# Kernel optimization log

Hardware: AMD Instinct MI355X
Metric: run time of the kernel (lower is better)

Reference implementation:

```python
import jax, jax.numpy as jnp
import numpy as np

K = 8  # 2^3 kernel offsets for kernel-size-2, stride-2 transposed conv in 3D (HYPER_CUBE)
HID = 64


def sp_convT(x, W, parent, kofs):
    """Sparse generative transposed conv via kernel map.
    x: [Nin, Cin]; W: [K, Cin, Cout]; parent: [Nout] int; kofs: [Nout] int in [0,K).
    out[j] = x[parent[j]] @ W[kofs[j]].
    """
    xg = x[parent]  # [Nout, Cin] gather
    out = jnp.zeros((parent.shape[0], W.shape[2]), dtype=x.dtype)
    for k in range(K):  # fixed small structural loop over kernel offsets
        out = out + jnp.where((kofs == k)[:, None], xg @ W[k], jnp.zeros((), x.dtype))
    return out


def setup_inputs() -> dict:
    key = jax.random.key(0)
    ks = jax.random.split(key, 12)
    Ns = [5000, 20000, 80000, 320000]
    sc_i = 1.0 / np.sqrt(64)
    inp = {
        'x0': jax.random.normal(ks[0], (Ns[0], 64), jnp.float32),
        'x1': jax.random.normal(ks[1], (Ns[1], 64), jnp.float32),
        'x2': jax.random.normal(ks[2], (Ns[2], 64), jnp.float32),
        'W_i': jax.random.normal(ks[3], (K, 64, 4 * HID), jnp.float32) * sc_i,
        'W_h': jax.random.normal(ks[4], (K, HID, 4 * HID), jnp.float32) * sc_i,
        'W_c': jax.random.normal(ks[5], (K, HID, HID), jnp.float32) * sc_i,
        'parent0': jax.random.randint(ks[6], (Ns[1],), 0, Ns[0], jnp.int32),
        'kofs0': jax.random.randint(ks[7], (Ns[1],), 0, K, jnp.int32),
        'parent1': jax.random.randint(ks[8], (Ns[2],), 0, Ns[1], jnp.int32),
        'kofs1': jax.random.randint(ks[9], (Ns[2],), 0, K, jnp.int32),
        'parent2': jax.random.randint(ks[10], (Ns[3],), 0, Ns[2], jnp.int32),
        'kofs2': jax.random.randint(ks[11], (Ns[3],), 0, K, jnp.int32),
    }
    return inp


def reference(x0, x1, x2, W_i, W_h, W_c, parent0, kofs0, parent1, kofs1, parent2, kofs2):
    xs = [x0, x1, x2]
    parents = [parent0, parent1, parent2]
    kofss = [kofs0, kofs1, kofs2]
    hx = jnp.zeros((x0.shape[0], HID), dtype=x0.dtype)
    cx = jnp.zeros((x0.shape[0], HID), dtype=x0.dtype)
    for t in range(3):  # coder_num timesteps (structural loop)
        p, ko = parents[t], kofss[t]
        cx = sp_convT(cx, W_c, p, ko)                                   # upsample cell state
        gates = sp_convT(hx, W_h, p, ko) + sp_convT(xs[t], W_i, p, ko)  # [Nout, 4*HID]
        in_g, fg, cg, og = jnp.split(gates, 4, axis=1)
        in_g = jax.nn.sigmoid(in_g)
        fg = jax.nn.sigmoid(fg)
        cg = jax.nn.sigmoid(cg)  # NOTE: original uses sigmoid (not tanh) for cell_gate
        og = jax.nn.sigmoid(og)
        cx = fg * cx + in_g * cg
        hx = og * jnp.tanh(cx)
    return hx
```

## Files before the change

kernel.cpp:

```cpp
#include <hip/hip_runtime.h>


#define KNUM 8
#define TM 32
#define STEP_THREADS 256

typedef __attribute__((ext_vector_type(8))) _Float16 f16x8;
typedef __attribute__((ext_vector_type(4))) float f32x4;

__device__ __forceinline__ float fsig(float x) {
  return __builtin_amdgcn_rcpf(1.0f + __expf(-x));
}
__device__ __forceinline__ float ftanh_(float x) {
  float e = __expf(2.0f * x);
  return 1.0f - 2.0f * __builtin_amdgcn_rcpf(e + 1.0f);
}
__device__ __forceinline__ f16x8 to_h8(float4 a, float4 b) {
  f16x8 r;
  r[0] = (_Float16)a.x; r[1] = (_Float16)a.y; r[2] = (_Float16)a.z; r[3] = (_Float16)a.w;
  r[4] = (_Float16)b.x; r[5] = (_Float16)b.y; r[6] = (_Float16)b.z; r[7] = (_Float16)b.w;
  return r;
}

__global__ void prep_kernel(const float* __restrict__ Wi, const float* __restrict__ Wh,
                            const float* __restrict__ Wc,
                            const float* __restrict__ x0, const float* __restrict__ x1,
                            const float* __restrict__ x2, int ne0, int ne1, int ne2,
                            _Float16* __restrict__ WgT, _Float16* __restrict__ WcT,
                            _Float16* __restrict__ x0f, _Float16* __restrict__ x1f,
                            _Float16* __restrict__ x2f,
                            int* __restrict__ counts, int* __restrict__ cursor) {
  int tid = blockIdx.x * blockDim.x + threadIdx.x;
  int stride = gridDim.x * blockDim.x;
  if (tid < 3 * KNUM) { counts[tid] = 0; cursor[tid] = 0; }
  for (int idx = tid; idx < KNUM * 256 * 128; idx += stride) {
    int k  = idx >> 15;
    int co = (idx >> 7) & 255;
    int ci = idx & 127;
    float v = (ci < 64) ? Wh[(k * 64 + ci) * 256 + co]
                        : Wi[(k * 64 + ci - 64) * 256 + co];
    WgT[idx] = (_Float16)v;
  }
  for (int idx = tid; idx < KNUM * 64 * 64; idx += stride) {
    int k  = idx >> 12;
    int co = (idx >> 6) & 63;
    int ci = idx & 63;
    WcT[idx] = (_Float16)Wc[(k * 64 + ci) * 64 + co];
  }
  for (int i = tid; i < (ne0 >> 3); i += stride) {
    float4 a = ((const float4*)x0)[2 * i], b = ((const float4*)x0)[2 * i + 1];
    ((f16x8*)x0f)[i] = to_h8(a, b);
  }
  for (int i = tid; i < (ne1 >> 3); i += stride) {
    float4 a = ((const float4*)x1)[2 * i], b = ((const float4*)x1)[2 * i + 1];
    ((f16x8*)x1f)[i] = to_h8(a, b);
  }
  for (int i = tid; i < (ne2 >> 3); i += stride) {
    float4 a = ((const float4*)x2)[2 * i], b = ((const float4*)x2)[2 * i + 1];
    ((f16x8*)x2f)[i] = to_h8(a, b);
  }
}

__device__ __forceinline__ void seg_select(int b, int& seg, int& rb, int& nb) {
  if (b < 32)       { seg = 0; rb = b;       nb = 32;  }
  else if (b < 160) { seg = 1; rb = b - 32;  nb = 128; }
  else              { seg = 2; rb = b - 160; nb = 352; }
}

__global__ void count_all_kernel(const int* __restrict__ k0, int n0,
                                 const int* __restrict__ k1, int n1,
                                 const int* __restrict__ k2, int n2,
                                 int* __restrict__ counts) {
  int seg, rb, nb;
  seg_select(blockIdx.x, seg, rb, nb);
  const int* kp = seg == 0 ? k0 : seg == 1 ? k1 : k2;
  int n = seg == 0 ? n0 : seg == 1 ? n1 : n2;
  int* cbase = counts + seg * KNUM;
  __shared__ int h[KNUM];
  if (threadIdx.x < KNUM) h[threadIdx.x] = 0;
  __syncthreads();
  for (int i = rb * blockDim.x + threadIdx.x; i < n; i += nb * blockDim.x)
    atomicAdd(&h[kp[i]], 1);
  __syncthreads();
  if (threadIdx.x < KNUM) atomicAdd(&cbase[threadIdx.x], h[threadIdx.x]);
}

__global__ void scatter_all_kernel(const int* __restrict__ k0, const int* __restrict__ p0, int n0,
                                   int* __restrict__ o0, int* __restrict__ q0,
                                   const int* __restrict__ k1, const int* __restrict__ p1, int n1,
                                   int* __restrict__ o1, int* __restrict__ q1,
                                   const int* __restrict__ k2, const int* __restrict__ p2, int n2,
                                   int* __restrict__ o2, int* __restrict__ q2,
                                   const int* __restrict__ counts, int* __restrict__ cursor) {
  int seg, rb, nb;
  seg_select(blockIdx.x, seg, rb, nb);
  const int* kp = seg == 0 ? k0 : seg == 1 ? k1 : k2;
  const int* pp = seg == 0 ? p0 : seg == 1 ? p1 : p2;
  int n = seg == 0 ? n0 : seg == 1 ? n1 : n2;
  int* order  = seg == 0 ? o0 : seg == 1 ? o1 : o2;
  int* porder = seg == 0 ? q0 : seg == 1 ? q1 : q2;

  __shared__ int h[KNUM], base[KNUM];
  if (threadIdx.x < KNUM) h[threadIdx.x] = 0;
  __syncthreads();
  int chunk = (n + nb - 1) / nb;
  int c0 = rb * chunk;
  int c1 = min(n, c0 + chunk);
  for (int i = c0 + threadIdx.x; i < c1; i += blockDim.x)
    atomicAdd(&h[kp[i]], 1);
  __syncthreads();
  if (threadIdx.x < KNUM) {
    int offk = 0;
    for (int k = 0; k < (int)threadIdx.x; ++k) offk += counts[seg * KNUM + k];
    base[threadIdx.x] = offk + atomicAdd(&cursor[seg * KNUM + threadIdx.x], h[threadIdx.x]);
    h[threadIdx.x] = 0;
  }
  __syncthreads();
  for (int i = c0 + threadIdx.x; i < c1; i += blockDim.x) {
    int k = kp[i];
    int pos = base[k] + atomicAdd(&h[k], 1);
    order[pos] = i;
    porder[pos] = pp[i];
  }
}

template <bool FIRST, bool LAST>
__global__ __launch_bounds__(STEP_THREADS)
void lstm_step_kernel(const _Float16* __restrict__ xf, const _Float16* __restrict__ h_in,
                      const _Float16* __restrict__ c_in,
                      const int* __restrict__ order, const int* __restrict__ porder,
                      const int* __restrict__ counts,
                      const _Float16* __restrict__ WgT, const _Float16* __restrict__ WcT,
                      float* __restrict__ out32, _Float16* __restrict__ h16,
                      _Float16* __restrict__ c16, int bpk) {
  __shared__ __align__(16) _Float16 A[TM][136];
  __shared__ __align__(16) _Float16 Cg[TM][72];
  __shared__ int jidx[TM];

  const int kb = blockIdx.x & 7;
  const int bi = blockIdx.x >> 3;
  int cnt = 0, off = 0;
#pragma unroll
  for (int k = 0; k < KNUM; ++k) {
    int c = counts[k];
    if (k < kb) off += c;
    if (k == kb) cnt = c;
  }
  const int ntiles = (cnt + TM - 1) / TM;
  if (bi >= ntiles) return;

  const int lane = threadIdx.x & 63;
  const int wc   = threadIdx.x >> 6;
  const int l15  = lane & 15;
  const int kg   = lane >> 4;

  f16x8 bg[4][4];
  f16x8 bc[2];
  {
    const _Float16* wgp = WgT + (size_t)kb * (256 * 128);
#pragma unroll
    for (int g = 0; g < 4; ++g)
#pragma unroll
      for (int ks = (FIRST ? 2 : 0); ks < 4; ++ks)
        bg[g][ks] = *(const f16x8*)(wgp + (size_t)(64 * g + 16 * wc + l15) * 128 + ks * 32 + kg * 8);
    if constexpr (!FIRST) {
      const _Float16* wcp = WcT + (size_t)kb * (64 * 64);
#pragma unroll
      for (int ks = 0; ks < 2; ++ks)
        bc[ks] = *(const f16x8*)(wcp + (size_t)(16 * wc + l15) * 64 + ks * 32 + kg * 8);
    }
  }

  const int gr  = threadIdx.x >> 3;
  const int gq8 = threadIdx.x & 7;

  int cj, cp; bool cv;
  int nj, np; bool nv;
  f16x8 sx{}, sh{}, sc{};

  auto idx_load = [&](int tt, int& j_, int& p_, bool& v_) {
    int grow = tt * TM + gr;
    v_ = (tt < ntiles) && (grow < cnt);
    j_ = -1; p_ = 0;
    if (v_) {
      if (gq8 == 0) j_ = order[off + grow];
      p_ = porder[off + grow];
    }
  };
  auto rows_load = [&](int p_, bool v_) {
    if (v_) {
      sx = *(const f16x8*)(xf + (size_t)p_ * 64 + gq8 * 8);
      if constexpr (!FIRST) {
        sh = *(const f16x8*)(h_in + (size_t)p_ * 64 + gq8 * 8);
        sc = *(const f16x8*)(c_in + (size_t)p_ * 64 + gq8 * 8);
      }
    } else {
      sx = f16x8{};
      if constexpr (!FIRST) { sh = f16x8{}; sc = f16x8{}; }
    }
  };

  idx_load(bi, cj, cp, cv);
  rows_load(cp, cv);
  idx_load(bi + bpk, nj, np, nv);

  for (int t = bi; t < ntiles; t += bpk) {
    __syncthreads();
    if (gq8 == 0) jidx[gr] = cj;
    *(f16x8*)&A[gr][64 + gq8 * 8] = sx;
    if constexpr (!FIRST) {
      *(f16x8*)&A[gr][gq8 * 8]  = sh;
      *(f16x8*)&Cg[gr][gq8 * 8] = sc;
    }
    __syncthreads();

    rows_load(np, nv);
    cj = nj;
    idx_load(t + 2 * bpk, nj, np, nv);

    f32x4 aG[2][4];
    f32x4 aC[2];
#pragma unroll
    for (int rf = 0; rf < 2; ++rf) {
#pragma unroll
      for (int g = 0; g < 4; ++g) aG[rf][g] = f32x4{0.f, 0.f, 0.f, 0.f};
      aC[rf] = f32x4{0.f, 0.f, 0.f, 0.f};
    }
#pragma unroll
    for (int ks = (FIRST ? 2 : 0); ks < 4; ++ks) {
#pragma unroll
      for (int rf = 0; rf < 2; ++rf) {
        f16x8 a = *(const f16x8*)&A[16 * rf + l15][ks * 32 + kg * 8];
        aG[rf][0] = __builtin_amdgcn_mfma_f32_16x16x32_f16(a, bg[0][ks], aG[rf][0], 0, 0, 0);
        aG[rf][1] = __builtin_amdgcn_mfma_f32_16x16x32_f16(a, bg[1][ks], aG[rf][1], 0, 0, 0);
        aG[rf][2] = __builtin_amdgcn_mfma_f32_16x16x32_f16(a, bg[2][ks], aG[rf][2], 0, 0, 0);
        aG[rf][3] = __builtin_amdgcn_mfma_f32_16x16x32_f16(a, bg[3][ks], aG[rf][3], 0, 0, 0);
      }
    }
    if constexpr (!FIRST) {
#pragma unroll
      for (int ks = 0; ks < 2; ++ks) {
#pragma unroll
        for (int rf = 0; rf < 2; ++rf) {
          f16x8 a = *(const f16x8*)&Cg[16 * rf + l15][ks * 32 + kg * 8];
          aC[rf] = __builtin_amdgcn_mfma_f32_16x16x32_f16(a, bc[ks], aC[rf], 0, 0, 0);
        }
      }
    }

#pragma unroll
    for (int rf = 0; rf < 2; ++rf) {
#pragma unroll
      for (int r = 0; r < 4; ++r) {
        int row = 16 * rf + kg * 4 + r;
        int j = jidx[row];
        if (j < 0) continue;
        float ing = fsig(aG[rf][0][r]);
        float fg  = fsig(aG[rf][1][r]);
        float cgt = fsig(aG[rf][2][r]);
        float og  = fsig(aG[rf][3][r]);
        float cup = FIRST ? 0.0f : aC[rf][r];
        float cxv = fg * cup + ing * cgt;
        float hxv = og * ftanh_(cxv);
        size_t o = (size_t)j * 64 + (16 * wc + l15);
        if constexpr (LAST) {
          out32[o] = hxv;
        } else {
          h16[o] = (_Float16)hxv;
          c16[o] = (_Float16)cxv;
        }
      }
    }
  }
}

static inline int idiv_up(int a, int b) { return (a + b - 1) / b; }

template <bool FIRST, bool LAST>
static void run_step(const _Float16* xf, const _Float16* h_in, const _Float16* c_in,
                     const int* order, const int* porder, int nout, const int* counts,
                     const _Float16* WgT, const _Float16* WcT,
                     float* out32, _Float16* h16, _Float16* c16, hipStream_t stream) {
  int bpk = idiv_up(nout, KNUM * TM);
  if (bpk > 128) bpk = 128;
  if (bpk < 1) bpk = 1;
  lstm_step_kernel<FIRST, LAST><<<dim3(KNUM * bpk), dim3(STEP_THREADS), 0, stream>>>(
      xf, h_in, c_in, order, porder, counts, WgT, WcT, out32, h16, c16, bpk);
}

extern "C" void kernel_launch(void* const* d_in, const int* in_sizes, int n_in,
                              void* d_out, int out_size, void* d_ws, size_t ws_size,
                              hipStream_t stream) {
  const float* x0 = (const float*)d_in[0];
  const float* x1 = (const float*)d_in[1];
  const float* x2 = (const float*)d_in[2];
  const float* Wi = (const float*)d_in[3];
  const float* Wh = (const float*)d_in[4];
  const float* Wc = (const float*)d_in[5];
  const int* parent0 = (const int*)d_in[6];
  const int* kofs0   = (const int*)d_in[7];
  const int* parent1 = (const int*)d_in[8];
  const int* kofs1   = (const int*)d_in[9];
  const int* parent2 = (const int*)d_in[10];
  const int* kofs2   = (const int*)d_in[11];
  const int N1 = in_sizes[6];
  const int N2 = in_sizes[8];
  const int N3 = in_sizes[10];
  const int ne0 = in_sizes[0], ne1 = in_sizes[1], ne2 = in_sizes[2];

  char* w = (char*)d_ws;
  auto carve = [&](size_t bytes) {
    char* p = w;
    w += (bytes + 255) & ~(size_t)255;
    return p;
  };
  _Float16* WgT = (_Float16*)carve((size_t)KNUM * 256 * 128 * 2);
  _Float16* WcT = (_Float16*)carve((size_t)KNUM * 64 * 64 * 2);
  int* counts   = (int*)carve(3 * KNUM * sizeof(int));
  int* cursor   = (int*)carve(3 * KNUM * sizeof(int));
  _Float16* x0f = (_Float16*)carve((size_t)ne0 * 2);
  _Float16* x1f = (_Float16*)carve((size_t)ne1 * 2);
  _Float16* x2f = (_Float16*)carve((size_t)ne2 * 2);
  int* ord0     = (int*)carve((size_t)N1 * sizeof(int));
  int* por0     = (int*)carve((size_t)N1 * sizeof(int));
  int* ord1     = (int*)carve((size_t)N2 * sizeof(int));
  int* por1     = (int*)carve((size_t)N2 * sizeof(int));
  int* ord2     = (int*)carve((size_t)N3 * sizeof(int));
  int* por2     = (int*)carve((size_t)N3 * sizeof(int));
  _Float16* h_a = (_Float16*)carve((size_t)N1 * 64 * 2);
  _Float16* c_a = (_Float16*)carve((size_t)N1 * 64 * 2);
  _Float16* h_b = (_Float16*)carve((size_t)N2 * 64 * 2);
  _Float16* c_b = (_Float16*)carve((size_t)N2 * 64 * 2);
  (void)ws_size; (void)n_in; (void)out_size;

  prep_kernel<<<1024, 256, 0, stream>>>(Wi, Wh, Wc, x0, x1, x2, ne0, ne1, ne2,
                                        WgT, WcT, x0f, x1f, x2f, counts, cursor);
  count_all_kernel<<<512, 256, 0, stream>>>(kofs0, N1, kofs1, N2, kofs2, N3, counts);
  scatter_all_kernel<<<512, 256, 0, stream>>>(kofs0, parent0, N1, ord0, por0,
                                              kofs1, parent1, N2, ord1, por1,
                                              kofs2, parent2, N3, ord2, por2,
                                              counts, cursor);

  run_step<true, false>(x0f, nullptr, nullptr, ord0, por0, N1, counts + 0 * KNUM,
                        WgT, WcT, nullptr, h_a, c_a, stream);
  run_step<false, false>(x1f, h_a, c_a, ord1, por1, N2, counts + 1 * KNUM,
                         WgT, WcT, nullptr, h_b, c_b, stream);
  run_step<false, true>(x2f, h_b, c_b, ord2, por2, N3, counts + 2 * KNUM,
                        WgT, WcT, (float*)d_out, nullptr, nullptr, stream);
}
```

Before: 118.7 us.

## Load MFMA A-fragments directly from global, drop LDS staging, fuse counting

The LSTM step kernel drops LDS staging and barriers. Each lane now gathers its MFMA A-operand fragments straight from global memory by parent index, and the tile size halves to 16 rows. Hidden and cell state are interleaved into one 128-wide fp16 buffer so one parent row is a single contiguous read. The count kernel is folded into the prep kernel and counters are zeroed with a memset, cutting a launch. The trade-off is redundant global loads of the same row by several waves, plus smaller tiles that give less weight reuse per tile.

```diff
diff --git a/kernel.cpp b/kernel.cpp
--- a/kernel.cpp
+++ b/kernel.cpp
@@ -2,7 +2,7 @@
 
 
 #define KNUM 8
-#define TM 32
+#define TM 16
 #define STEP_THREADS 256
 
 typedef __attribute__((ext_vector_type(8))) _Float16 f16x8;
@@ -26,13 +26,17 @@
                             const float* __restrict__ Wc,
                             const float* __restrict__ x0, const float* __restrict__ x1,
                             const float* __restrict__ x2, int ne0, int ne1, int ne2,
+                            const int* __restrict__ k0, int n0,
+                            const int* __restrict__ k1, int n1,
+                            const int* __restrict__ k2, int n2,
                             _Float16* __restrict__ WgT, _Float16* __restrict__ WcT,
                             _Float16* __restrict__ x0f, _Float16* __restrict__ x1f,
-                            _Float16* __restrict__ x2f,
-                            int* __restrict__ counts, int* __restrict__ cursor) {
+                            _Float16* __restrict__ x2f, int* __restrict__ counts) {
+  __shared__ int sh[3 * KNUM];
+  if (threadIdx.x < 3 * KNUM) sh[threadIdx.x] = 0;
+  __syncthreads();
   int tid = blockIdx.x * blockDim.x + threadIdx.x;
   int stride = gridDim.x * blockDim.x;
-  if (tid < 3 * KNUM) { counts[tid] = 0; cursor[tid] = 0; }
   for (int idx = tid; idx < KNUM * 256 * 128; idx += stride) {
     int k  = idx >> 15;
     int co = (idx >> 7) & 255;
@@ -59,30 +63,17 @@
     float4 a = ((const float4*)x2)[2 * i], b = ((const float4*)x2)[2 * i + 1];
     ((f16x8*)x2f)[i] = to_h8(a, b);
   }
+  for (int i = tid; i < n0; i += stride) atomicAdd(&sh[k0[i]], 1);
+  for (int i = tid; i < n1; i += stride) atomicAdd(&sh[KNUM + k1[i]], 1);
+  for (int i = tid; i < n2; i += stride) atomicAdd(&sh[2 * KNUM + k2[i]], 1);
+  __syncthreads();
+  if (threadIdx.x < 3 * KNUM && sh[threadIdx.x]) atomicAdd(&counts[threadIdx.x], sh[threadIdx.x]);
 }
 
 __device__ __forceinline__ void seg_select(int b, int& seg, int& rb, int& nb) {
   if (b < 32)       { seg = 0; rb = b;       nb = 32;  }
   else if (b < 160) { seg = 1; rb = b - 32;  nb = 128; }
   else              { seg = 2; rb = b - 160; nb = 352; }
-}
-
-__global__ void count_all_kernel(const int* __restrict__ k0, int n0,
-                                 const int* __restrict__ k1, int n1,
-                                 const int* __restrict__ k2, int n2,
-                                 int* __restrict__ counts) {
-  int seg, rb, nb;
-  seg_select(blockIdx.x, seg, rb, nb);
-  const int* kp = seg == 0 ? k0 : seg == 1 ? k1 : k2;
-  int n = seg == 0 ? n0 : seg == 1 ? n1 : n2;
-  int* cbase = counts + seg * KNUM;
-  __shared__ int h[KNUM];
-  if (threadIdx.x < KNUM) h[threadIdx.x] = 0;
-  __syncthreads();
-  for (int i = rb * blockDim.x + threadIdx.x; i < n; i += nb * blockDim.x)
-    atomicAdd(&h[kp[i]], 1);
-  __syncthreads();
-  if (threadIdx.x < KNUM) atomicAdd(&cbase[threadIdx.x], h[threadIdx.x]);
 }
 
 __global__ void scatter_all_kernel(const int* __restrict__ k0, const int* __restrict__ p0, int n0,
@@ -126,16 +117,12 @@
 
 template <bool FIRST, bool LAST>
 __global__ __launch_bounds__(STEP_THREADS)
-void lstm_step_kernel(const _Float16* __restrict__ xf, const _Float16* __restrict__ h_in,
-                      const _Float16* __restrict__ c_in,
+void lstm_step_kernel(const _Float16* __restrict__ xf, const _Float16* __restrict__ hc_in,
                       const int* __restrict__ order, const int* __restrict__ porder,
                       const int* __restrict__ counts,
                       const _Float16* __restrict__ WgT, const _Float16* __restrict__ WcT,
-                      float* __restrict__ out32, _Float16* __restrict__ h16,
-                      _Float16* __restrict__ c16, int bpk) {
-  __shared__ __align__(16) _Float16 A[TM][136];
-  __shared__ __align__(16) _Float16 Cg[TM][72];
-  __shared__ int jidx[TM];
+                      float* __restrict__ out32, _Float16* __restrict__ hc_out, int bpk) {
+  constexpr int NKS = FIRST ? 2 : 4;
 
   const int kb = blockIdx.x & 7;
   const int bi = blockIdx.x >> 3;
@@ -154,122 +141,104 @@
   const int l15  = lane & 15;
   const int kg   = lane >> 4;
 
-  f16x8 bg[4][4];
+  f16x8 bg[4][NKS];
   f16x8 bc[2];
   {
-    const _Float16* wgp = WgT + (size_t)kb * (256 * 128);
+    const _Float16* wgp = WgT + (size_t)kb * (256 * 128) + kg * 8 + (FIRST ? 64 : 0);
 #pragma unroll
     for (int g = 0; g < 4; ++g)
 #pragma unroll
-      for (int ks = (FIRST ? 2 : 0); ks < 4; ++ks)
-        bg[g][ks] = *(const f16x8*)(wgp + (size_t)(64 * g + 16 * wc + l15) * 128 + ks * 32 + kg * 8);
+      for (int s = 0; s < NKS; ++s)
+        bg[g][s] = *(const f16x8*)(wgp + (size_t)(64 * g + 16 * wc + l15) * 128 + s * 32);
     if constexpr (!FIRST) {
-      const _Float16* wcp = WcT + (size_t)kb * (64 * 64);
-#pragma unroll
-      for (int ks = 0; ks < 2; ++ks)
-        bc[ks] = *(const f16x8*)(wcp + (size_t)(16 * wc + l15) * 64 + ks * 32 + kg * 8);
-    }
-  }
-
-  const int gr  = threadIdx.x >> 3;
-  const int gq8 = threadIdx.x & 7;
-
-  int cj, cp; bool cv;
-  int nj, np; bool nv;
-  f16x8 sx{}, sh{}, sc{};
-
-  auto idx_load = [&](int tt, int& j_, int& p_, bool& v_) {
-    int grow = tt * TM + gr;
-    v_ = (tt < ntiles) && (grow < cnt);
-    j_ = -1; p_ = 0;
-    if (v_) {
-      if (gq8 == 0) j_ = order[off + grow];
-      p_ = porder[off + grow];
+      const _Float16* wcp = WcT + (size_t)kb * (64 * 64) + kg * 8;
+#pragma unroll
+      for (int s = 0; s < 2; ++s)
+        bc[s] = *(const f16x8*)(wcp + (size_t)(16 * wc + l15) * 64 + s * 32);
+    }
+  }
+
+  auto idx_of = [&](int t, int& p, int* j) {
+    int tt = min(t, ntiles - 1);
+    int base = tt * TM;
+    p = porder[off + min(base + l15, cnt - 1)];
+#pragma unroll
+    for (int r = 0; r < 4; ++r) {
+      int grow = base + kg * 4 + r;
+      j[r] = (t < ntiles && grow < cnt) ? order[off + grow] : -1;
     }
   };
-  auto rows_load = [&](int p_, bool v_) {
-    if (v_) {
-      sx = *(const f16x8*)(xf + (size_t)p_ * 64 + gq8 * 8);
-      if constexpr (!FIRST) {
-        sh = *(const f16x8*)(h_in + (size_t)p_ * 64 + gq8 * 8);
-        sc = *(const f16x8*)(c_in + (size_t)p_ * 64 + gq8 * 8);
+  auto frags_of = [&](int p, f16x8* fx, f16x8* fh, f16x8* fc) {
+    const _Float16* xr = xf + (size_t)p * 64 + kg * 8;
+    fx[0] = *(const f16x8*)(xr);
+    fx[1] = *(const f16x8*)(xr + 32);
+    if constexpr (!FIRST) {
+      const _Float16* hr = hc_in + (size_t)p * 128 + kg * 8;
+      fh[0] = *(const f16x8*)(hr);
+      fh[1] = *(const f16x8*)(hr + 32);
+      fc[0] = *(const f16x8*)(hr + 64);
+      fc[1] = *(const f16x8*)(hr + 96);
+    }
+  };
+
+  int pc, jc[4], pn, jn[4];
+  f16x8 cfx[2], cfh[2], cfc[2];
+  f16x8 nfx[2], nfh[2], nfc[2];
+
+  idx_of(bi, pc, jc);
+  frags_of(pc, cfx, cfh, cfc);
+
+  for (int t = bi; t < ntiles; t += bpk) {
+    idx_of(t + bpk, pn, jn);
+    frags_of(pn, nfx, nfh, nfc);
+
+    f32x4 aG[4];
+    f32x4 aC;
+#pragma unroll
+    for (int g = 0; g < 4; ++g) aG[g] = f32x4{0.f, 0.f, 0.f, 0.f};
+    aC = f32x4{0.f, 0.f, 0.f, 0.f};
+#pragma unroll
+    for (int s = 0; s < NKS; ++s) {
+      f16x8 a;
+      if constexpr (FIRST) a = cfx[s];
+      else a = (s < 2) ? cfh[s] : cfx[s - 2];
+      aG[0] = __builtin_amdgcn_mfma_f32_16x16x32_f16(a, bg[0][s], aG[0], 0, 0, 0);
+      aG[1] = __builtin_amdgcn_mfma_f32_16x16x32_f16(a, bg[1][s], aG[1], 0, 0, 0);
+      aG[2] = __builtin_amdgcn_mfma_f32_16x16x32_f16(a, bg[2][s], aG[2], 0, 0, 0);
+      aG[3] = __builtin_amdgcn_mfma_f32_16x16x32_f16(a, bg[3][s], aG[3], 0, 0, 0);
+    }
+    if constexpr (!FIRST) {
+      aC = __builtin_amdgcn_mfma_f32_16x16x32_f16(cfc[0], bc[0], aC, 0, 0, 0);
+      aC = __builtin_amdgcn_mfma_f32_16x16x32_f16(cfc[1], bc[1], aC, 0, 0, 0);
+    }
+
+#pragma unroll
+    for (int r = 0; r < 4; ++r) {
+      int j = jc[r];
+      if (j < 0) continue;
+      float ing = fsig(aG[0][r]);
+      float fg  = fsig(aG[1][r]);
+      float cgt = fsig(aG[2][r]);
+      float og  = fsig(aG[3][r]);
+      float cup = FIRST ? 0.0f : aC[r];
+      float cxv = fg * cup + ing * cgt;
+      float hxv = og * ftanh_(cxv);
+      int ch = 16 * wc + l15;
+      if constexpr (LAST) {
+        out32[(size_t)j * 64 + ch] = hxv;
+      } else {
+        hc_out[(size_t)j * 128 + ch]      = (_Float16)hxv;
+        hc_out[(size_t)j * 128 + 64 + ch] = (_Float16)cxv;
       }
-    } else {
-      sx = f16x8{};
-      if constexpr (!FIRST) { sh = f16x8{}; sc = f16x8{}; }
-    }
-  };
-
-  idx_load(bi, cj, cp, cv);
-  rows_load(cp, cv);
-  idx_load(bi + bpk, nj, np, nv);
-
-  for (int t = bi; t < ntiles; t += bpk) {
-    __syncthreads();
-    if (gq8 == 0) jidx[gr] = cj;
-    *(f16x8*)&A[gr][64 + gq8 * 8] = sx;
-    if constexpr (!FIRST) {
-      *(f16x8*)&A[gr][gq8 * 8]  = sh;
-      *(f16x8*)&Cg[gr][gq8 * 8] = sc;
-    }
-    __syncthreads();
-
-    rows_load(np, nv);
-    cj = nj;
-    idx_load(t + 2 * bpk, nj, np, nv);
-
-    f32x4 aG[2][4];
-    f32x4 aC[2];
-#pragma unroll
-    for (int rf = 0; rf < 2; ++rf) {
-#pragma unroll
-      for (int g = 0; g < 4; ++g) aG[rf][g] = f32x4{0.f, 0.f, 0.f, 0.f};
-      aC[rf] = f32x4{0.f, 0.f, 0.f, 0.f};
-    }
-#pragma unroll
-    for (int ks = (FIRST ? 2 : 0); ks < 4; ++ks) {
-#pragma unroll
-      for (int rf = 0; rf < 2; ++rf) {
-        f16x8 a = *(const f16x8*)&A[16 * rf + l15][ks * 32 + kg * 8];
-        aG[rf][0] = __builtin_amdgcn_mfma_f32_16x16x32_f16(a, bg[0][ks], aG[rf][0], 0, 0, 0);
-        aG[rf][1] = __builtin_amdgcn_mfma_f32_16x16x32_f16(a, bg[1][ks], aG[rf][1], 0, 0, 0);
-        aG[rf][2] = __builtin_amdgcn_mfma_f32_16x16x32_f16(a, bg[2][ks], aG[rf][2], 0, 0, 0);
-        aG[rf][3] = __builtin_amdgcn_mfma_f32_16x16x32_f16(a, bg[3][ks], aG[rf][3], 0, 0, 0);
-      }
-    }
-    if constexpr (!FIRST) {
-#pragma unroll
-      for (int ks = 0; ks < 2; ++ks) {
-#pragma unroll
-        for (int rf = 0; rf < 2; ++rf) {
-          f16x8 a = *(const f16x8*)&Cg[16 * rf + l15][ks * 32 + kg * 8];
-          aC[rf] = __builtin_amdgcn_mfma_f32_16x16x32_f16(a, bc[ks], aC[rf], 0, 0, 0);
-        }
-      }
-    }
-
-#pragma unroll
-    for (int rf = 0; rf < 2; ++rf) {
-#pragma unroll
-      for (int r = 0; r < 4; ++r) {
-        int row = 16 * rf + kg * 4 + r;
-        int j = jidx[row];
-        if (j < 0) continue;
-        float ing = fsig(aG[rf][0][r]);
-        float fg  = fsig(aG[rf][1][r]);
-        float cgt = fsig(aG[rf][2][r]);
-        float og  = fsig(aG[rf][3][r]);
-        float cup = FIRST ? 0.0f : aC[rf][r];
-        float cxv = fg * cup + ing * cgt;
-        float hxv = og * ftanh_(cxv);
-        size_t o = (size_t)j * 64 + (16 * wc + l15);
-        if constexpr (LAST) {
-          out32[o] = hxv;
-        } else {
-          h16[o] = (_Float16)hxv;
-          c16[o] = (_Float16)cxv;
-        }
-      }
+    }
+
+    pc = pn;
+#pragma unroll
+    for (int r = 0; r < 4; ++r) jc[r] = jn[r];
+#pragma unroll
+    for (int s = 0; s < 2; ++s) {
+      cfx[s] = nfx[s];
+      if constexpr (!FIRST) { cfh[s] = nfh[s]; cfc[s] = nfc[s]; }
     }
   }
 }
@@ -277,15 +246,15 @@
 static inline int idiv_up(int a, int b) { return (a + b - 1) / b; }
 
 template <bool FIRST, bool LAST>
-static void run_step(const _Float16* xf, const _Float16* h_in, const _Float16* c_in,
+static void run_step(const _Float16* xf, const _Float16* hc_in,
                      const int* order, const int* porder, int nout, const int* counts,
                      const _Float16* WgT, const _Float16* WcT,
-                     float* out32, _Float16* h16, _Float16* c16, hipStream_t stream) {
+                     float* out32, _Float16* hc_out, hipStream_t stream) {
   int bpk = idiv_up(nout, KNUM * TM);
   if (bpk > 128) bpk = 128;
   if (bpk < 1) bpk = 1;
   lstm_step_kernel<FIRST, LAST><<<dim3(KNUM * bpk), dim3(STEP_THREADS), 0, stream>>>(
-      xf, h_in, c_in, order, porder, counts, WgT, WcT, out32, h16, c16, bpk);
+      xf, hc_in, order, porder, counts, WgT, WcT, out32, hc_out, bpk);
 }
 
 extern "C" void kernel_launch(void* const* d_in, const int* in_sizes, int n_in,
@@ -316,8 +285,9 @@
   };
   _Float16* WgT = (_Float16*)carve((size_t)KNUM * 256 * 128 * 2);
   _Float16* WcT = (_Float16*)carve((size_t)KNUM * 64 * 64 * 2);
-  int* counts   = (int*)carve(3 * KNUM * sizeof(int));
-  int* cursor   = (int*)carve(3 * KNUM * sizeof(int));
+  int* ctrs     = (int*)carve(6 * KNUM * sizeof(int));
+  int* counts   = ctrs;
+  int* cursor   = ctrs + 3 * KNUM;
   _Float16* x0f = (_Float16*)carve((size_t)ne0 * 2);
   _Float16* x1f = (_Float16*)carve((size_t)ne1 * 2);
   _Float16* x2f = (_Float16*)carve((size_t)ne2 * 2);
@@ -327,24 +297,23 @@
   int* por1     = (int*)carve((size_t)N2 * sizeof(int));
   int* ord2     = (int*)carve((size_t)N3 * sizeof(int));
   int* por2     = (int*)carve((size_t)N3 * sizeof(int));
-  _Float16* h_a = (_Float16*)carve((size_t)N1 * 64 * 2);
-  _Float16* c_a = (_Float16*)carve((size_t)N1 * 64 * 2);
-  _Float16* h_b = (_Float16*)carve((size_t)N2 * 64 * 2);
-  _Float16* c_b = (_Float16*)carve((size_t)N2 * 64 * 2);
+  _Float16* hc_a = (_Float16*)carve((size_t)N1 * 128 * 2);
+  _Float16* hc_b = (_Float16*)carve((size_t)N2 * 128 * 2);
   (void)ws_size; (void)n_in; (void)out_size;
 
+  hipMemsetAsync(ctrs, 0, 6 * KNUM * sizeof(int), stream);
   prep_kernel<<<1024, 256, 0, stream>>>(Wi, Wh, Wc, x0, x1, x2, ne0, ne1, ne2,
-                                        WgT, WcT, x0f, x1f, x2f, counts, cursor);
-  count_all_kernel<<<512, 256, 0, stream>>>(kofs0, N1, kofs1, N2, kofs2, N3, counts);
+                                        kofs0, N1, kofs1, N2, kofs2, N3,
+                                        WgT, WcT, x0f, x1f, x2f, counts);
   scatter_all_kernel<<<512, 256, 0, stream>>>(kofs0, parent0, N1, ord0, por0,
                                               kofs1, parent1, N2, ord1, por1,
                                               kofs2, parent2, N3, ord2, por2,
                                               counts, cursor);
 
-  run_step<true, false>(x0f, nullptr, nullptr, ord0, por0, N1, counts + 0 * KNUM,
-                        WgT, WcT, nullptr, h_a, c_a, stream);
-  run_step<false, false>(x1f, h_a, c_a, ord1, por1, N2, counts + 1 * KNUM,
-                         WgT, WcT, nullptr, h_b, c_b, stream);
-  run_step<false, true>(x2f, h_b, c_b, ord2, por2, N3, counts + 2 * KNUM,
-                        WgT, WcT, (float*)d_out, nullptr, nullptr, stream);
-}
+  run_step<true, false>(x0f, nullptr, ord0, por0, N1, counts + 0 * KNUM,
+                        WgT, WcT, nullptr, hc_a, stream);
+  run_step<false, false>(x1f, hc_a, ord1, por1, N2, counts + 1 * KNUM,
+                         WgT, WcT, nullptr, hc_b, stream);
+  run_step<false, true>(x2f, hc_b, ord2, por2, N3, counts + 2 * KNUM,
+                        WgT, WcT, (float*)d_out, nullptr, stream);
+}
```

After: 170.7 us. 1.44x slower.

## Bucket rows by offset and parent region, interleave h/c state, fuse counting into prep

Applied to the files above, without the earlier changes.

Rows are now sorted into buckets keyed by kernel offset and a coarse parent-index region, so parent gathers within a tile hit nearby memory and cache better. Hidden and cell state are stored interleaved in one buffer, so a single row fetch covers both. The histogram is built inside the prep kernel, a small scan kernel computes the bucket offsets, the count kernel and in-kernel prefix loop are removed, and counters are cleared with a memset. The weight transpose loops now read the source contiguously and write strided, and the per-offset block cap is raised. This adds a kernel launch and a larger shared histogram with more atomics in prep.

```diff
diff --git a/kernel.cpp b/kernel.cpp
--- a/kernel.cpp
+++ b/kernel.cpp
@@ -2,6 +2,8 @@
 
 
 #define KNUM 8
+#define NREG 64
+#define NBUK (KNUM * NREG)
 #define TM 32
 #define STEP_THREADS 256
 
@@ -26,26 +28,31 @@
                             const float* __restrict__ Wc,
                             const float* __restrict__ x0, const float* __restrict__ x1,
                             const float* __restrict__ x2, int ne0, int ne1, int ne2,
+                            const int* __restrict__ k0, const int* __restrict__ p0, int n0,
+                            const int* __restrict__ k1, const int* __restrict__ p1, int n1,
+                            const int* __restrict__ k2, const int* __restrict__ p2, int n2,
+                            int s0, int s1, int s2,
                             _Float16* __restrict__ WgT, _Float16* __restrict__ WcT,
                             _Float16* __restrict__ x0f, _Float16* __restrict__ x1f,
-                            _Float16* __restrict__ x2f,
-                            int* __restrict__ counts, int* __restrict__ cursor) {
+                            _Float16* __restrict__ x2f, int* __restrict__ counts) {
+  __shared__ int hist[3 * NBUK];
+  for (int i = threadIdx.x; i < 3 * NBUK; i += blockDim.x) hist[i] = 0;
+  __syncthreads();
   int tid = blockIdx.x * blockDim.x + threadIdx.x;
   int stride = gridDim.x * blockDim.x;
-  if (tid < 3 * KNUM) { counts[tid] = 0; cursor[tid] = 0; }
-  for (int idx = tid; idx < KNUM * 256 * 128; idx += stride) {
+  for (int idx = tid; idx < KNUM * 128 * 256; idx += stride) {
     int k  = idx >> 15;
-    int co = (idx >> 7) & 255;
-    int ci = idx & 127;
+    int ci = (idx >> 8) & 127;
+    int co = idx & 255;
     float v = (ci < 64) ? Wh[(k * 64 + ci) * 256 + co]
                         : Wi[(k * 64 + ci - 64) * 256 + co];
-    WgT[idx] = (_Float16)v;
+    WgT[((size_t)k * 256 + co) * 128 + ci] = (_Float16)v;
   }
   for (int idx = tid; idx < KNUM * 64 * 64; idx += stride) {
     int k  = idx >> 12;
-    int co = (idx >> 6) & 63;
-    int ci = idx & 63;
-    WcT[idx] = (_Float16)Wc[(k * 64 + ci) * 64 + co];
+    int ci = (idx >> 6) & 63;
+    int co = idx & 63;
+    WcT[((size_t)k * 64 + co) * 64 + ci] = (_Float16)Wc[(k * 64 + ci) * 64 + co];
   }
   for (int i = tid; i < (ne0 >> 3); i += stride) {
     float4 a = ((const float4*)x0)[2 * i], b = ((const float4*)x0)[2 * i + 1];
@@ -58,6 +65,34 @@
   for (int i = tid; i < (ne2 >> 3); i += stride) {
     float4 a = ((const float4*)x2)[2 * i], b = ((const float4*)x2)[2 * i + 1];
     ((f16x8*)x2f)[i] = to_h8(a, b);
+  }
+  for (int i = tid; i < n0; i += stride)
+    atomicAdd(&hist[k0[i] * NREG + min(p0[i] >> s0, NREG - 1)], 1);
+  for (int i = tid; i < n1; i += stride)
+    atomicAdd(&hist[NBUK + k1[i] * NREG + min(p1[i] >> s1, NREG - 1)], 1);
+  for (int i = tid; i < n2; i += stride)
+    atomicAdd(&hist[2 * NBUK + k2[i] * NREG + min(p2[i] >> s2, NREG - 1)], 1);
+  __syncthreads();
+  for (int i = threadIdx.x; i < 3 * NBUK; i += blockDim.x)
+    if (hist[i]) atomicAdd(&counts[i], hist[i]);
+}
+
+__global__ void scan_kernel(const int* __restrict__ counts, int* __restrict__ offsets) {
+  __shared__ int buf[NBUK];
+  for (int s = 0; s < 3; ++s) {
+    int v = counts[s * NBUK + threadIdx.x];
+    buf[threadIdx.x] = v;
+    __syncthreads();
+    int sum = v;
+    for (int d = 1; d < NBUK; d <<= 1) {
+      int add = (threadIdx.x >= (unsigned)d) ? buf[threadIdx.x - d] : 0;
+      __syncthreads();
+      sum += add;
+      buf[threadIdx.x] = sum;
+      __syncthreads();
+    }
+    offsets[s * NBUK + threadIdx.x] = sum - v;
+    __syncthreads();
   }
 }
 
@@ -65,24 +100,6 @@
   if (b < 32)       { seg = 0; rb = b;       nb = 32;  }
   else if (b < 160) { seg = 1; rb = b - 32;  nb = 128; }
   else              { seg = 2; rb = b - 160; nb = 352; }
-}
-
-__global__ void count_all_kernel(const int* __restrict__ k0, int n0,
-                                 const int* __restrict__ k1, int n1,
-                                 const int* __restrict__ k2, int n2,
-                                 int* __restrict__ counts) {
-  int seg, rb, nb;
-  seg_select(blockIdx.x, seg, rb, nb);
-  const int* kp = seg == 0 ? k0 : seg == 1 ? k1 : k2;
-  int n = seg == 0 ? n0 : seg == 1 ? n1 : n2;
-  int* cbase = counts + seg * KNUM;
-  __shared__ int h[KNUM];
-  if (threadIdx.x < KNUM) h[threadIdx.x] = 0;
-  __syncthreads();
-  for (int i = rb * blockDim.x + threadIdx.x; i < n; i += nb * blockDim.x)
-    atomicAdd(&h[kp[i]], 1);
-  __syncthreads();
-  if (threadIdx.x < KNUM) atomicAdd(&cbase[threadIdx.x], h[threadIdx.x]);
 }
 
 __global__ void scatter_all_kernel(const int* __restrict__ k0, const int* __restrict__ p0, int n0,
@@ -91,34 +108,37 @@
                                    int* __restrict__ o1, int* __restrict__ q1,
                                    const int* __restrict__ k2, const int* __restrict__ p2, int n2,
                                    int* __restrict__ o2, int* __restrict__ q2,
-                                   const int* __restrict__ counts, int* __restrict__ cursor) {
+                                   int s0, int s1, int s2,
+                                   const int* __restrict__ offsets, int* __restrict__ cursor) {
   int seg, rb, nb;
   seg_select(blockIdx.x, seg, rb, nb);
   const int* kp = seg == 0 ? k0 : seg == 1 ? k1 : k2;
   const int* pp = seg == 0 ? p0 : seg == 1 ? p1 : p2;
-  int n = seg == 0 ? n0 : seg == 1 ? n1 : n2;
+  int n  = seg == 0 ? n0 : seg == 1 ? n1 : n2;
+  int sh = seg == 0 ? s0 : seg == 1 ? s1 : s2;
   int* order  = seg == 0 ? o0 : seg == 1 ? o1 : o2;
   int* porder = seg == 0 ? q0 : seg == 1 ? q1 : q2;
 
-  __shared__ int h[KNUM], base[KNUM];
-  if (threadIdx.x < KNUM) h[threadIdx.x] = 0;
+  __shared__ int h[NBUK], base[NBUK];
+  for (int i = threadIdx.x; i < NBUK; i += blockDim.x) h[i] = 0;
   __syncthreads();
   int chunk = (n + nb - 1) / nb;
   int c0 = rb * chunk;
   int c1 = min(n, c0 + chunk);
-  for (int i = c0 + threadIdx.x; i < c1; i += blockDim.x)
-    atomicAdd(&h[kp[i]], 1);
-  __syncthreads();
-  if (threadIdx.x < KNUM) {
-    int offk = 0;
-    for (int k = 0; k < (int)threadIdx.x; ++k) offk += counts[seg * KNUM + k];
-    base[threadIdx.x] = offk + atomicAdd(&cursor[seg * KNUM + threadIdx.x], h[threadIdx.x]);
-    h[threadIdx.x] = 0;
-  }
-  __syncthreads();
   for (int i = c0 + threadIdx.x; i < c1; i += blockDim.x) {
-    int k = kp[i];
-    int pos = base[k] + atomicAdd(&h[k], 1);
+    int b = kp[i] * NREG + min(pp[i] >> sh, NREG - 1);
+    atomicAdd(&h[b], 1);
+  }
+  __syncthreads();
+  for (int b = threadIdx.x; b < NBUK; b += blockDim.x) {
+    base[b] = offsets[seg * NBUK + b] +
+              (h[b] ? atomicAdd(&cursor[seg * NBUK + b], h[b]) : 0);
+    h[b] = 0;
+  }
+  __syncthreads();
+  for (int i = c0 + threadIdx.x; i < c1; i += blockDim.x) {
+    int b = kp[i] * NREG + min(pp[i] >> sh, NREG - 1);
+    int pos = base[b] + atomicAdd(&h[b], 1);
     order[pos] = i;
     porder[pos] = pp[i];
   }
@@ -126,26 +146,20 @@
 
 template <bool FIRST, bool LAST>
 __global__ __launch_bounds__(STEP_THREADS)
-void lstm_step_kernel(const _Float16* __restrict__ xf, const _Float16* __restrict__ h_in,
-                      const _Float16* __restrict__ c_in,
+void lstm_step_kernel(const _Float16* __restrict__ xf, const _Float16* __restrict__ hc_in,
                       const int* __restrict__ order, const int* __restrict__ porder,
-                      const int* __restrict__ counts,
+                      const int* __restrict__ offsets, int n,
                       const _Float16* __restrict__ WgT, const _Float16* __restrict__ WcT,
-                      float* __restrict__ out32, _Float16* __restrict__ h16,
-                      _Float16* __restrict__ c16, int bpk) {
+                      float* __restrict__ out32, _Float16* __restrict__ hc_out, int bpk) {
   __shared__ __align__(16) _Float16 A[TM][136];
   __shared__ __align__(16) _Float16 Cg[TM][72];
   __shared__ int jidx[TM];
 
   const int kb = blockIdx.x & 7;
   const int bi = blockIdx.x >> 3;
-  int cnt = 0, off = 0;
-#pragma unroll
-  for (int k = 0; k < KNUM; ++k) {
-    int c = counts[k];
-    if (k < kb) off += c;
-    if (k == kb) cnt = c;
-  }
+  const int off = offsets[kb * NREG];
+  const int nxt = (kb < KNUM - 1) ? offsets[(kb + 1) * NREG] : n;
+  const int cnt = nxt - off;
   const int ntiles = (cnt + TM - 1) / TM;
   if (bi >= ntiles) return;
 
@@ -191,8 +205,9 @@
     if (v_) {
       sx = *(const f16x8*)(xf + (size_t)p_ * 64 + gq8 * 8);
       if constexpr (!FIRST) {
-        sh = *(const f16x8*)(h_in + (size_t)p_ * 64 + gq8 * 8);
-        sc = *(const f16x8*)(c_in + (size_t)p_ * 64 + gq8 * 8);
+        const _Float16* hr = hc_in + (size_t)p_ * 128 + gq8 * 8;
+        sh = *(const f16x8*)(hr);
+        sc = *(const f16x8*)(hr + 64);
       }
     } else {
       sx = f16x8{};
@@ -262,12 +277,12 @@
         float cup = FIRST ? 0.0f : aC[rf][r];
         float cxv = fg * cup + ing * cgt;
         float hxv = og * ftanh_(cxv);
-        size_t o = (size_t)j * 64 + (16 * wc + l15);
+        int ch = 16 * wc + l15;
         if constexpr (LAST) {
-          out32[o] = hxv;
+          out32[(size_t)j * 64 + ch] = hxv;
         } else {
-          h16[o] = (_Float16)hxv;
-          c16[o] = (_Float16)cxv;
+          hc_out[(size_t)j * 128 + ch]      = (_Float16)hxv;
+          hc_out[(size_t)j * 128 + 64 + ch] = (_Float16)cxv;
         }
       }
     }
@@ -277,15 +292,15 @@
 static inline int idiv_up(int a, int b) { return (a + b - 1) / b; }
 
 template <bool FIRST, bool LAST>
-static void run_step(const _Float16* xf, const _Float16* h_in, const _Float16* c_in,
-                     const int* order, const int* porder, int nout, const int* counts,
+static void run_step(const _Float16* xf, const _Float16* hc_in,
+                     const int* order, const int* porder, int nout, const int* offsets,
                      const _Float16* WgT, const _Float16* WcT,
-                     float* out32, _Float16* h16, _Float16* c16, hipStream_t stream) {
+                     float* out32, _Float16* hc_out, hipStream_t stream) {
   int bpk = idiv_up(nout, KNUM * TM);
-  if (bpk > 128) bpk = 128;
+  if (bpk > 256) bpk = 256;
   if (bpk < 1) bpk = 1;
   lstm_step_kernel<FIRST, LAST><<<dim3(KNUM * bpk), dim3(STEP_THREADS), 0, stream>>>(
-      xf, h_in, c_in, order, porder, counts, WgT, WcT, out32, h16, c16, bpk);
+      xf, hc_in, order, porder, offsets, nout, WgT, WcT, out32, hc_out, bpk);
 }
 
 extern "C" void kernel_launch(void* const* d_in, const int* in_sizes, int n_in,
@@ -307,6 +322,10 @@
   const int N2 = in_sizes[8];
   const int N3 = in_sizes[10];
   const int ne0 = in_sizes[0], ne1 = in_sizes[1], ne2 = in_sizes[2];
+  const int nin0 = ne0 / 64, nin1 = ne1 / 64, nin2 = ne2 / 64;
+
+  auto shf = [](int nin) { int s = 0; while ((nin >> s) > NREG) ++s; return s; };
+  const int s0 = shf(nin0), s1 = shf(nin1), s2 = shf(nin2);
 
   char* w = (char*)d_ws;
   auto carve = [&](size_t bytes) {
@@ -316,8 +335,10 @@
   };
   _Float16* WgT = (_Float16*)carve((size_t)KNUM * 256 * 128 * 2);
   _Float16* WcT = (_Float16*)carve((size_t)KNUM * 64 * 64 * 2);
-  int* counts   = (int*)carve(3 * KNUM * sizeof(int));
-  int* cursor   = (int*)carve(3 * KNUM * sizeof(int));
+  int* ctrs     = (int*)carve(6 * NBUK * sizeof(int));
+  int* counts   = ctrs;
+  int* cursor   = ctrs + 3 * NBUK;
+  int* offsets  = (int*)carve(3 * NBUK * sizeof(int));
   _Float16* x0f = (_Float16*)carve((size_t)ne0 * 2);
   _Float16* x1f = (_Float16*)carve((size_t)ne1 * 2);
   _Float16* x2f = (_Float16*)carve((size_t)ne2 * 2);
@@ -327,24 +348,25 @@
   int* por1     = (int*)carve((size_t)N2 * sizeof(int));
   int* ord2     = (int*)carve((size_t)N3 * sizeof(int));
   int* por2     = (int*)carve((size_t)N3 * sizeof(int));
-  _Float16* h_a = (_Float16*)carve((size_t)N1 * 64 * 2);
-  _Float16* c_a = (_Float16*)carve((size_t)N1 * 64 * 2);
-  _Float16* h_b = (_Float16*)carve((size_t)N2 * 64 * 2);
-  _Float16* c_b = (_Float16*)carve((size_t)N2 * 64 * 2);
+  _Float16* hc_a = (_Float16*)carve((size_t)N1 * 128 * 2);
+  _Float16* hc_b = (_Float16*)carve((size_t)N2 * 128 * 2);
   (void)ws_size; (void)n_in; (void)out_size;
 
+  hipMemsetAsync(ctrs, 0, 6 * NBUK * sizeof(int), stream);
   prep_kernel<<<1024, 256, 0, stream>>>(Wi, Wh, Wc, x0, x1, x2, ne0, ne1, ne2,
-                                        WgT, WcT, x0f, x1f, x2f, counts, cursor);
-  count_all_kernel<<<512, 256, 0, stream>>>(kofs0, N1, kofs1, N2, kofs2, N3, counts);
+                                        kofs0, parent0, N1, kofs1, parent1, N2,
+                                        kofs2, parent2, N3, s0, s1, s2,
+                                        WgT, WcT, x0f, x1f, x2f, counts);
+  scan_kernel<<<1, NBUK, 0, stream>>>(counts, offsets);
   scatter_all_kernel<<<512, 256, 0, stream>>>(kofs0, parent0, N1, ord0, por0,
                                               kofs1, parent1, N2, ord1, por1,
                                               kofs2, parent2, N3, ord2, por2,
-                                              counts, cursor);
-
-  run_step<true, false>(x0f, nullptr, nullptr, ord0, por0, N1, counts + 0 * KNUM,
-                        WgT, WcT, nullptr, h_a, c_a, stream);
-  run_step<false, false>(x1f, h_a, c_a, ord1, por1, N2, counts + 1 * KNUM,
-                         WgT, WcT, nullptr, h_b, c_b, stream);
-  run_step<false, true>(x2f, h_b, c_b, ord2, por2, N3, counts + 2 * KNUM,
-                        WgT, WcT, (float*)d_out, nullptr, nullptr, stream);
-}
+                                              s0, s1, s2, offsets, cursor);
+
+  run_step<true, false>(x0f, nullptr, ord0, por0, N1, offsets + 0 * NBUK,
+                        WgT, WcT, nullptr, hc_a, stream);
+  run_step<false, false>(x1f, hc_a, ord1, por1, N2, offsets + 1 * NBUK,
+                         WgT, WcT, nullptr, hc_b, stream);
+  run_step<false, true>(x2f, hc_b, ord2, por2, N3, offsets + 2 * NBUK,
+                        WgT, WcT, (float*)d_out, nullptr, stream);
+}
```

New measurement: 151.4 us. 1.28x slower.
